# Kernel optimization log

Measured on AMD Instinct MI355X. Metric: run time of the kernel, lower is better.

## Reference

```python
import jax, jax.numpy as jnp
import numpy as np
from math import factorial, sqrt

MUL = 64            # common multiplicity of all irreps
BASE = 9            # base_dim for 0e+1o+2e = 1+3+5
LS = [0, 1, 2]      # l of each base irrep
OFFS = [0, 1, 4]    # offset of each base irrep inside base_dim
INSTR = [(0,0,0),(0,1,1),(0,2,2),(1,0,1),(1,1,0),(1,1,2),(1,2,1),(2,0,2),(2,1,1),(2,2,0),(2,2,2)]
Z = 50000           # number of edges (batch)


def _w3j_complex(l1, l2, l3):
    # Racah formula for the (complex-basis) Wigner 3j symbol.
    f = factorial
    W = np.zeros((2*l1+1, 2*l2+1, 2*l3+1))
    delta = sqrt(f(l1+l2-l3)*f(l1-l2+l3)*f(-l1+l2+l3)/f(l1+l2+l3+1))
    for m1 in range(-l1, l1+1):
        for m2 in range(-l2, l2+1):
            m3 = -m1 - m2
            if abs(m3) > l3:
                continue
            pre = (-1)**(l1-l2-m3) * delta * sqrt(
                f(l1+m1)*f(l1-m1)*f(l2+m2)*f(l2-m2)*f(l3+m3)*f(l3-m3))
            s = 0.0
            for t in range(0, l1+l2-l3+1):
                dens = [t, l3-l2+t+m1, l3-l1+t-m2, l1+l2-l3-t, l1-t-m1, l2-t+m2]
                if any(d < 0 for d in dens):
                    continue
                s += (-1)**t / np.prod([float(f(d)) for d in dens])
            W[m1+l1, m2+l2, m3+l3] = pre * s
    return W


def _c2r(l):
    # complex->real spherical harmonic change of basis
    U = np.zeros((2*l+1, 2*l+1), dtype=complex)
    U[l, l] = 1.0
    s2 = 1.0/sqrt(2.0)
    for m in range(1, l+1):
        U[l+m, l+m] = (-1)**m * s2
        U[l+m, l-m] = s2
        U[l-m, l-m] = 1j * s2
        U[l-m, l+m] = -1j * (-1)**m * s2
    return U


def _w3j_real(l1, l2, l3):
    C = _w3j_complex(l1, l2, l3).astype(complex)
    R = np.einsum('ax,by,cz,xyz->abc', _c2r(l1), _c2r(l2), _c2r(l3), C)
    # real if l1+l2+l3 even, purely imaginary otherwise
    return R.real if np.abs(R.real).max() >= np.abs(R.imag).max() else R.imag


def _build_w3j():
    # dense buffer of shape (num_paths, k_out, i_in1, j_in2) with CG blocks
    P = len(INSTR)
    W = np.zeros((P, BASE, BASE, BASE), dtype=np.float32)
    counts = {}
    for ins in INSTR:
        counts[ins[2]] = counts.get(ins[2], 0) + 1
    for p, (i1, i2, io) in enumerate(INSTR):
        l1, l2, lo = LS[i1], LS[i2], LS[io]
        blk = _w3j_real(l1, l2, lo)  # (2l1+1, 2l2+1, 2lo+1)
        # 'component' normalization, 'uuu' mode: alpha = sqrt((2*lo+1)/n_paths_to_out)
        alpha = sqrt((2*lo+1) / counts[io])
        o1, o2, oo = OFFS[i1], OFFS[i2], OFFS[io]
        W[p, oo:oo+2*lo+1, o1:o1+2*l1+1, o2:o2+2*l2+1] = alpha * blk.transpose(2, 0, 1)
    return jnp.asarray(W)


def setup_inputs() -> dict:
    key = jax.random.key(0)
    k1, k2, k3 = jax.random.split(key, 3)
    x1 = jax.random.normal(k1, (Z, MUL*BASE), dtype=jnp.float32)
    x2 = jax.random.normal(k2, (Z, MUL*BASE), dtype=jnp.float32)
    # 'uniform' init -> unit-variance uniform on [-sqrt(3), sqrt(3)], shape (mul, num_paths)
    weights = jax.random.uniform(k3, (MUL, len(INSTR)), dtype=jnp.float32,
                                 minval=-sqrt(3.0), maxval=sqrt(3.0))
    return {"x1": x1, "x2": x2, "weights": weights, "w3j": _build_w3j()}


def reference(x1, x2, weights, w3j):
    x1 = x1.reshape(-1, MUL, BASE)   # (z, u, i)
    x2 = x2.reshape(-1, MUL, BASE)   # (z, u, j)
    # 'up,pkij->ukij' : fold per-channel per-path weights into the CG tensor
    ww3j = jnp.einsum('up,pkij->ukij', weights, w3j)
    # 'zui,zuj,ukij->zuk' : channel-wise bilinear CG contraction
    return jnp.einsum('zui,zuj,ukij->zuk', x1, x2, ww3j)
```

## Files before the change

### kernel.cpp

```cpp
#include <hip/hip_runtime.h>


#define MUL   64
#define BASE  9
#define NPATH 11
#define ZT    64

__global__ __launch_bounds__(256) void fold_kernel(
    const float* __restrict__ weights,
    const float* __restrict__ w3j,
    float*       __restrict__ ww)
{
    int u = blockIdx.x / 3;
    int t = (blockIdx.x % 3) * 256 + threadIdx.x;
    if (t >= 729) return;
    float acc = 0.f;
#pragma unroll
    for (int p = 0; p < NPATH; ++p)
        acc = fmaf(weights[u * NPATH + p], w3j[p * 729 + t], acc);
    ww[u * 729 + t] = acc;
}

__global__ __launch_bounds__(256) void tp_kernel(
    const float* __restrict__ x1,
    const float* __restrict__ x2,
    const float* __restrict__ ww,
    float*       __restrict__ out,
    int Z, int n_zt)
{
    int b    = blockIdx.x;
    int xcd  = b & 7;
    int j    = b >> 3;
    int uc   = j & 15;
    int q    = j >> 4;
    int zt   = xcd + 8 * q;
    if (zt >= n_zt) return;

    int wave = threadIdx.x >> 6;
    int lane = threadIdx.x & 63;
    int u    = __builtin_amdgcn_readfirstlane(uc * 4 + wave);
    int z    = zt * ZT + lane;
    bool active = (z < Z);

    const float* __restrict__ wrow = ww + u * 729;

    const float* p1 = x1 + (size_t)z * 576 + u * 9;
    const float* p2 = x2 + (size_t)z * 576 + u * 9;

    float X1[BASE], X2[BASE];
#pragma unroll
    for (int i = 0; i < BASE; ++i) {
        X1[i] = active ? p1[i] : 0.f;
        X2[i] = active ? p2[i] : 0.f;
    }

    float r[BASE * BASE];
#pragma unroll
    for (int i = 0; i < BASE; ++i)
#pragma unroll
        for (int jj = 0; jj < BASE; ++jj)
            r[i * BASE + jj] = X1[i] * X2[jj];

    float o[BASE];
#pragma unroll
    for (int k = 0; k < BASE; ++k) o[k] = 0.f;
#pragma unroll
    for (int t = 0; t < BASE * BASE; ++t)
#pragma unroll
        for (int k = 0; k < BASE; ++k)
            o[k] = fmaf(wrow[k * 81 + t], r[t], o[k]);

    float* po = out + (size_t)z * 576 + u * 9;
    if (active) {
#pragma unroll
        for (int k = 0; k < BASE; ++k) po[k] = o[k];
    }
}

extern "C" void kernel_launch(void* const* d_in, const int* in_sizes, int n_in,
                              void* d_out, int out_size, void* d_ws, size_t ws_size,
                              hipStream_t stream) {
    const float* x1  = (const float*)d_in[0];
    const float* x2  = (const float*)d_in[1];
    const float* w   = (const float*)d_in[2];
    const float* w3j = (const float*)d_in[3];
    float* out = (float*)d_out;
    float* ww  = (float*)d_ws;

    int Z = in_sizes[0] / (MUL * BASE);

    fold_kernel<<<MUL * 3, 256, 0, stream>>>(w, w3j, ww);

    int n_zt = (Z + ZT - 1) / ZT;
    int Q    = (n_zt + 7) / 8;
    int grid = 8 * 16 * Q;
    tp_kernel<<<grid, 256, 0, stream>>>(x1, x2, ww, out, Z, n_zt);
}
```

Baseline: 317.4 us.

## Stage x1/x2 tiles through LDS with coalesced float4 loads and swizzled layout

```diff
diff --git a/kernel.cpp b/kernel.cpp
--- a/kernel.cpp
+++ b/kernel.cpp
@@ -5,6 +5,9 @@
 #define BASE  9
 #define NPATH 11
 #define ZT    64
+#define UC    8
+#define TW    (UC * BASE)
+#define NF4   (ZT * TW / 4)
 
 __global__ __launch_bounds__(256) void fold_kernel(
     const float* __restrict__ weights,
@@ -21,59 +24,116 @@
     ww[u * 729 + t] = acc;
 }
 
-__global__ __launch_bounds__(256) void tp_kernel(
+__global__ __launch_bounds__(256, 4) void tp_kernel(
     const float* __restrict__ x1,
     const float* __restrict__ x2,
     const float* __restrict__ ww,
     float*       __restrict__ out,
     int Z, int n_zt)
 {
-    int b    = blockIdx.x;
-    int xcd  = b & 7;
-    int j    = b >> 3;
-    int uc   = j & 15;
-    int q    = j >> 4;
-    int zt   = xcd + 8 * q;
+    __shared__ float s1[ZT * TW];
+    __shared__ float s2[ZT * TW];
+
+    int b   = blockIdx.x;
+    int xcd = b & 7;
+    int t   = b >> 3;
+    int uc  = t & 7;
+    int q   = t >> 3;
+    int zt  = xcd + 8 * q;
     if (zt >= n_zt) return;
 
-    int wave = threadIdx.x >> 6;
-    int lane = threadIdx.x & 63;
-    int u    = __builtin_amdgcn_readfirstlane(uc * 4 + wave);
-    int z    = zt * ZT + lane;
-    bool active = (z < Z);
+    int tid  = threadIdx.x;
+    int wave = tid >> 6;
+    int lane = tid & 63;
 
-    const float* __restrict__ wrow = ww + u * 729;
+    const size_t gbase = (size_t)zt * ZT * 576 + (size_t)uc * TW;
 
-    const float* p1 = x1 + (size_t)z * 576 + u * 9;
-    const float* p2 = x2 + (size_t)z * 576 + u * 9;
+#pragma unroll
+    for (int rep = 0; rep < 5; ++rep) {
+        int f = rep * 256 + tid;
+        if (f < NF4) {
+            int r  = f / 18;
+            int c4 = f % 18;
+            int z  = zt * ZT + r;
+            float4 v1 = make_float4(0.f, 0.f, 0.f, 0.f);
+            float4 v2 = make_float4(0.f, 0.f, 0.f, 0.f);
+            if (z < Z) {
+                const size_t g = gbase + (size_t)r * 576 + c4 * 4;
+                v1 = *(const float4*)(x1 + g);
+                v2 = *(const float4*)(x2 + g);
+            }
+            int a    = (r >> 2) & 7;
+            int base = r * TW;
+            int c    = c4 * 4;
+            s1[base + ((c + 0) ^ a)] = v1.x;
+            s1[base + ((c + 1) ^ a)] = v1.y;
+            s1[base + ((c + 2) ^ a)] = v1.z;
+            s1[base + ((c + 3) ^ a)] = v1.w;
+            s2[base + ((c + 0) ^ a)] = v2.x;
+            s2[base + ((c + 1) ^ a)] = v2.y;
+            s2[base + ((c + 2) ^ a)] = v2.z;
+            s2[base + ((c + 3) ^ a)] = v2.w;
+        }
+    }
+    __syncthreads();
 
-    float X1[BASE], X2[BASE];
+    int az   = (lane >> 2) & 7;
+    int zrow = lane * TW;
 #pragma unroll
-    for (int i = 0; i < BASE; ++i) {
-        X1[i] = active ? p1[i] : 0.f;
-        X2[i] = active ? p2[i] : 0.f;
-    }
+    for (int it = 0; it < 2; ++it) {
+        int du = wave * 2 + it;
+        int u  = __builtin_amdgcn_readfirstlane(uc * UC + du);
+        const float* __restrict__ wrow = ww + u * 729;
 
-    float r[BASE * BASE];
+        float X1[BASE], X2[BASE];
 #pragma unroll
-    for (int i = 0; i < BASE; ++i)
+        for (int i = 0; i < BASE; ++i) {
+            int c = du * BASE + i;
+            X1[i] = s1[zrow + (c ^ az)];
+            X2[i] = s2[zrow + (c ^ az)];
+        }
+
+        float r_[BASE * BASE];
 #pragma unroll
-        for (int jj = 0; jj < BASE; ++jj)
-            r[i * BASE + jj] = X1[i] * X2[jj];
+        for (int i = 0; i < BASE; ++i)
+#pragma unroll
+            for (int j = 0; j < BASE; ++j)
+                r_[i * BASE + j] = X1[i] * X2[j];
 
-    float o[BASE];
+        float o[BASE];
 #pragma unroll
-    for (int k = 0; k < BASE; ++k) o[k] = 0.f;
+        for (int k = 0; k < BASE; ++k) o[k] = 0.f;
 #pragma unroll
-    for (int t = 0; t < BASE * BASE; ++t)
+        for (int tt = 0; tt < BASE * BASE; ++tt)
+#pragma unroll
+            for (int k = 0; k < BASE; ++k)
+                o[k] = fmaf(wrow[k * 81 + tt], r_[tt], o[k]);
+
 #pragma unroll
         for (int k = 0; k < BASE; ++k)
-            o[k] = fmaf(wrow[k * 81 + t], r[t], o[k]);
+            s1[zrow + ((du * BASE + k) ^ az)] = o[k];
+    }
+    __syncthreads();
 
-    float* po = out + (size_t)z * 576 + u * 9;
-    if (active) {
 #pragma unroll
-        for (int k = 0; k < BASE; ++k) po[k] = o[k];
+    for (int rep = 0; rep < 5; ++rep) {
+        int f = rep * 256 + tid;
+        if (f < NF4) {
+            int r  = f / 18;
+            int c4 = f % 18;
+            int z  = zt * ZT + r;
+            if (z < Z) {
+                int a    = (r >> 2) & 7;
+                int base = r * TW;
+                int c    = c4 * 4;
+                float4 v;
+                v.x = s1[base + ((c + 0) ^ a)];
+                v.y = s1[base + ((c + 1) ^ a)];
+                v.z = s1[base + ((c + 2) ^ a)];
+                v.w = s1[base + ((c + 3) ^ a)];
+                *(float4*)(out + gbase + (size_t)r * 576 + c4 * 4) = v;
+            }
+        }
     }
 }
 
@@ -93,6 +153,6 @@
 
     int n_zt = (Z + ZT - 1) / ZT;
     int Q    = (n_zt + 7) / 8;
-    int grid = 8 * 16 * Q;
+    int grid = 8 * 8 * Q;
     tp_kernel<<<grid, 256, 0, stream>>>(x1, x2, ww, out, Z, n_zt);
 }
```

After: 407.9 us. +28.5%, slower.

## Exploit CG sparsity and stage coalesced rows through LDS in persistent kernel

Applied to the files above, without the earlier changes.

```diff
diff --git a/kernel.cpp b/kernel.cpp
--- a/kernel.cpp
+++ b/kernel.cpp
@@ -1,79 +1,141 @@
 #include <hip/hip_runtime.h>
 
 
-#define MUL   64
-#define BASE  9
-#define NPATH 11
-#define ZT    64
+#define MUL    64
+#define BASE   9
+#define NPATH  11
+#define NNZ    83
+#define RPC    2
+#define STRIDE 584
+#define SFL    (RPC * STRIDE)
+#define F4T    (RPC * 576 / 4)
 
-__global__ __launch_bounds__(256) void fold_kernel(
+constexpr unsigned char cK[NNZ] = {
+    0,
+    1,2,3,
+    4,5,6,7,8,
+    1,2,3,
+    0,0,0,
+    4,4,5,5,6,6,6,7,7,8,8,
+    3,1,2,1,1,2,3,3,2,1,3,
+    4,5,6,7,8,
+    3,1,2,1,1,2,3,3,2,1,3,
+    0,0,0,0,0,
+    6,6,8,6,6,8,6, 7,7, 4,4, 5,5, 5,5, 4,4, 5,5, 7,7, 8,8, 7,7};
+constexpr unsigned char cI[NNZ] = {
+    0,
+    0,0,0,
+    0,0,0,0,0,
+    1,2,3,
+    1,2,3,
+    1,3,1,2,1,2,3,2,3,1,3,
+    1,3,1,2,1,2,3,2,3,1,3,
+    4,5,6,7,8,
+    4,4,5,5,6,6,6,7,7,8,8,
+    4,5,6,7,8,
+    4,5,5,6,7,7,8, 4,5, 4,6, 4,7, 5,6, 5,7, 5,8, 6,7, 6,8, 7,8};
+constexpr unsigned char cJ[NNZ] = {
+    0,
+    1,2,3,
+    4,5,6,7,8,
+    0,0,0,
+    1,2,3,
+    3,1,2,1,1,2,3,3,2,1,3,
+    4,4,5,5,6,6,6,7,7,8,8,
+    0,0,0,0,0,
+    1,3,1,2,1,2,3,2,3,1,3,
+    4,5,6,7,8,
+    4,5,5,6,7,7,8, 5,4, 6,4, 7,4, 6,5, 7,5, 8,5, 7,6, 8,6, 8,7};
+
+__global__ __launch_bounds__(256) void pack_kernel(
     const float* __restrict__ weights,
     const float* __restrict__ w3j,
-    float*       __restrict__ ww)
+    float*       __restrict__ wws)
 {
-    int u = blockIdx.x / 3;
-    int t = (blockIdx.x % 3) * 256 + threadIdx.x;
-    if (t >= 729) return;
+    int t = blockIdx.x * 256 + threadIdx.x;
+    if (t >= NNZ * MUL) return;
+    int n = t >> 6;
+    int u = t & 63;
+    int idx = cK[n] * 81 + cI[n] * 9 + cJ[n];
     float acc = 0.f;
 #pragma unroll
     for (int p = 0; p < NPATH; ++p)
-        acc = fmaf(weights[u * NPATH + p], w3j[p * 729 + t], acc);
-    ww[u * 729 + t] = acc;
+        acc = fmaf(weights[u * NPATH + p], w3j[p * 729 + idx], acc);
+    wws[t] = acc;
 }
 
 __global__ __launch_bounds__(256) void tp_kernel(
     const float* __restrict__ x1,
     const float* __restrict__ x2,
-    const float* __restrict__ ww,
+    const float* __restrict__ wws,
     float*       __restrict__ out,
-    int Z, int n_zt)
+    int Z, int nchunks)
 {
-    int b    = blockIdx.x;
-    int xcd  = b & 7;
-    int j    = b >> 3;
-    int uc   = j & 15;
-    int q    = j >> 4;
-    int zt   = xcd + 8 * q;
-    if (zt >= n_zt) return;
+    __shared__ float lds[4 * 2 * SFL];
 
     int wave = threadIdx.x >> 6;
     int lane = threadIdx.x & 63;
-    int u    = __builtin_amdgcn_readfirstlane(uc * 4 + wave);
-    int z    = zt * ZT + lane;
-    bool active = (z < Z);
+    float* s1 = lds + wave * (2 * SFL);
+    float* s2 = s1 + SFL;
 
-    const float* __restrict__ wrow = ww + u * 729;
+    float wwr[NNZ];
+#pragma unroll
+    for (int n = 0; n < NNZ; ++n) wwr[n] = wws[n * MUL + lane];
 
-    const float* p1 = x1 + (size_t)z * 576 + u * 9;
-    const float* p2 = x2 + (size_t)z * 576 + u * 9;
+    int stride = gridDim.x * 4;
 
-    float X1[BASE], X2[BASE];
+    for (int c = blockIdx.x * 4 + wave; c < nchunks; c += stride) {
+        size_t base = (size_t)c * (RPC * 576);
+
 #pragma unroll
-    for (int i = 0; i < BASE; ++i) {
-        X1[i] = active ? p1[i] : 0.f;
-        X2[i] = active ? p2[i] : 0.f;
-    }
+        for (int t = 0; t < 5; ++t) {
+            int f = t * 64 + lane;
+            if (f < F4T) {
+                int rr = f / 144;
+                int z  = c * RPC + rr;
+                float4 v1 = make_float4(0.f, 0.f, 0.f, 0.f);
+                float4 v2 = make_float4(0.f, 0.f, 0.f, 0.f);
+                if (z < Z) {
+                    v1 = *(const float4*)(x1 + base + f * 4);
+                    v2 = *(const float4*)(x2 + base + f * 4);
+                }
+                int off = f * 4 + 8 * rr;
+                *(float4*)(s1 + off) = v1;
+                *(float4*)(s2 + off) = v2;
+            }
+        }
 
-    float r[BASE * BASE];
 #pragma unroll
-    for (int i = 0; i < BASE; ++i)
+        for (int r = 0; r < RPC; ++r) {
+            int bo = r * STRIDE + lane * 9;
+            float X1v[BASE], X2v[BASE];
 #pragma unroll
-        for (int jj = 0; jj < BASE; ++jj)
-            r[i * BASE + jj] = X1[i] * X2[jj];
+            for (int i = 0; i < BASE; ++i) {
+                X1v[i] = s1[bo + i];
+                X2v[i] = s2[bo + i];
+            }
+            float o[BASE];
+#pragma unroll
+            for (int k = 0; k < BASE; ++k) o[k] = 0.f;
+#pragma unroll
+            for (int n = 0; n < NNZ; ++n)
+                o[cK[n]] = fmaf(wwr[n], X1v[cI[n]] * X2v[cJ[n]], o[cK[n]]);
+#pragma unroll
+            for (int k = 0; k < BASE; ++k) s1[bo + k] = o[k];
+        }
 
-    float o[BASE];
 #pragma unroll
-    for (int k = 0; k < BASE; ++k) o[k] = 0.f;
-#pragma unroll
-    for (int t = 0; t < BASE * BASE; ++t)
-#pragma unroll
-        for (int k = 0; k < BASE; ++k)
-            o[k] = fmaf(wrow[k * 81 + t], r[t], o[k]);
-
-    float* po = out + (size_t)z * 576 + u * 9;
-    if (active) {
-#pragma unroll
-        for (int k = 0; k < BASE; ++k) po[k] = o[k];
+        for (int t = 0; t < 5; ++t) {
+            int f = t * 64 + lane;
+            if (f < F4T) {
+                int rr = f / 144;
+                int z  = c * RPC + rr;
+                if (z < Z) {
+                    int off = f * 4 + 8 * rr;
+                    *(float4*)(out + base + f * 4) = *(const float4*)(s1 + off);
+                }
+            }
+        }
     }
 }
 
@@ -85,14 +147,12 @@
     const float* w   = (const float*)d_in[2];
     const float* w3j = (const float*)d_in[3];
     float* out = (float*)d_out;
-    float* ww  = (float*)d_ws;
+    float* wws = (float*)d_ws;
 
     int Z = in_sizes[0] / (MUL * BASE);
 
-    fold_kernel<<<MUL * 3, 256, 0, stream>>>(w, w3j, ww);
+    pack_kernel<<<(NNZ * MUL + 255) / 256, 256, 0, stream>>>(w, w3j, wws);
 
-    int n_zt = (Z + ZT - 1) / ZT;
-    int Q    = (n_zt + 7) / 8;
-    int grid = 8 * 16 * Q;
-    tp_kernel<<<grid, 256, 0, stream>>>(x1, x2, ww, out, Z, n_zt);
+    int nchunks = (Z + RPC - 1) / RPC;
+    tp_kernel<<<1024, 256, 0, stream>>>(x1, x2, wws, out, Z, nchunks);
 }
```

Result: faster. 287.0 us (-9.6%).
